# Kernel optimization log

Hardware: AMD Instinct MI355X
Metric: run time of the kernel (lower is better)

The kernel has to match this reference:

```python
import jax, jax.numpy as jnp
import numpy as np

B, C, S = 16, 8, 128
DT, DX, DY = 0.001, 1.0, 1.0
NUM_STEPS = 10
EPS = 1e-6


def _thomas(a, b, c, d):
    """Batched Thomas tridiagonal solve. a,b,c,d: [M,N] rows; solve along N."""
    aT, bT, cT, dT = a.T, b.T, c.T, d.T  # [N, M]
    zero = jnp.zeros_like(dT[0])

    def fwd(carry, inp):
        cs_p, ds_p = carry
        ai, bi, ci, di = inp
        denom = bi - ai * cs_p + EPS  # i=0: cs_p=0 -> denom = b0 + eps (matches torch)
        cs = ci / denom
        ds = (di - ai * ds_p) / denom
        return (cs, ds), (cs, ds)

    _, (c_star, d_star) = jax.lax.scan(fwd, (zero, zero), (aT, bT, cT, dT))

    def bwd(x_next, inp):
        ci, di = inp
        x = di - ci * x_next
        return x, x

    _, xs = jax.lax.scan(bwd, d_star[-1], (c_star[:-1], d_star[:-1]), reverse=True)
    x = jnp.concatenate([xs, d_star[-1:]], axis=0)  # [N, M]
    return x.T


def _diffuse_rows(u2d, coeff):
    """Implicit 1D diffusion along last axis. u2d, coeff: [M,N]."""
    a = -coeff
    c = -coeff
    b = 1.0 + 2.0 * coeff
    b = b.at[:, 0].set(1.0 + coeff[:, 0])
    b = b.at[:, -1].set(1.0 + coeff[:, -1])
    return _thomas(a, b, c, u2d)


def _forward(u, alpha_base, beta_base, alpha_time_coeff, beta_time_coeff, channel_mixing):
    Bb, Cc, H, W = u.shape
    half = DT / 2.0
    t = 0.0
    for _ in range(NUM_STEPS):
        # x half-step (coefficient alpha at time t)
        alpha = jnp.clip(alpha_base + alpha_time_coeff * t, EPS, 10.0)
        u = jnp.einsum('dc,bchw->bdhw', channel_mixing, u)
        uf = u.reshape(Bb * Cc, H, W)
        af = jnp.broadcast_to(alpha[None], (Bb, Cc, H, W)).reshape(Bb * Cc, H, W)
        uf = _diffuse_rows(uf.reshape(-1, W), af.reshape(-1, W) * half / DX**2).reshape(Bb * Cc, H, W)
        t += half
        # y full step (coefficient beta at time t+dt/2)
        beta = jnp.clip(beta_base + beta_time_coeff * t, EPS, 10.0)
        bf = jnp.broadcast_to(beta[None], (Bb, Cc, H, W)).reshape(Bb * Cc, H, W)
        ut = uf.transpose(0, 2, 1).reshape(-1, H)
        bt = bf.transpose(0, 2, 1).reshape(-1, H)
        ut = _diffuse_rows(ut, bt * DT / DY**2)
        uf = ut.reshape(Bb * Cc, W, H).transpose(0, 2, 1)
        t += half
        # x half-step (coefficient alpha at time t+dt)
        alpha = jnp.clip(alpha_base + alpha_time_coeff * t, EPS, 10.0)
        af = jnp.broadcast_to(alpha[None], (Bb, Cc, H, W)).reshape(Bb * Cc, H, W)
        uf = _diffuse_rows(uf.reshape(-1, W), af.reshape(-1, W) * half / DX**2).reshape(Bb * Cc, H, W)
        u = uf.reshape(Bb, Cc, H, W)
    return u


def setup_inputs() -> dict:
    key = jax.random.key(0)
    k_u, k_cm, k_atc, k_btc = jax.random.split(key, 4)
    u = jax.random.normal(k_u, (B, C, S, S), dtype=jnp.float32)
    alpha_base = jnp.ones((C, S, S), dtype=jnp.float32)
    beta_base = jnp.ones((C, S, S), dtype=jnp.float32)
    alpha_time_coeff = jax.random.normal(k_atc, (C, S, S), dtype=jnp.float32) * 0.01
    beta_time_coeff = jax.random.normal(k_btc, (C, S, S), dtype=jnp.float32) * 0.01
    channel_mixing = jnp.eye(C, dtype=jnp.float32) + jax.random.normal(k_cm, (C, C), dtype=jnp.float32) * 0.01
    return {
        'u': u,
        'alpha_base': alpha_base,
        'beta_base': beta_base,
        'alpha_time_coeff': alpha_time_coeff,
        'beta_time_coeff': beta_time_coeff,
        'channel_mixing': channel_mixing,
    }


def reference(u, alpha_base, beta_base, alpha_time_coeff, beta_time_coeff, channel_mixing):
    return _forward(u, alpha_base, beta_base, alpha_time_coeff, beta_time_coeff, channel_mixing)
```

## Files before the change

kernel.cpp:

```cpp
#include <hip/hip_runtime.h>


constexpr int S_ = 128;
constexpr int RS = 129;
constexpr float EPSF = 1e-6f;

constexpr int OFF_A = 0;
constexpr int OFF_B = 12384;
constexpr int OFF_C = 24768;
constexpr int POOL  = 33024;

__device__ __forceinline__ void jrun(const float (&e)[12], const float (&g)[12],
                                     float (&o)[8]) {
    float x1[12];
    #pragma unroll
    for (int i = 1; i <= 10; ++i) x1[i] = fmaf(g[i], e[i - 1] + e[i + 1], e[i]);
    #pragma unroll
    for (int i = 2; i <= 9; ++i) o[i - 2] = fmaf(g[i], x1[i - 1] + x1[i + 1], e[i]);
}

template <bool HEAD, bool TAILMIX>
__global__ __launch_bounds__(512, 2) void step_kernel(
    const float* __restrict__ usrc, float* __restrict__ udst,
    const float* __restrict__ ab, const float* __restrict__ atc,
    const float* __restrict__ bbeta, const float* __restrict__ btc,
    const float* __restrict__ cm, float t_y, float t_x)
{
    __shared__ float sP[POOL];
    const int tid = threadIdx.x;
    const int b   = blockIdx.x >> 4;
    const int h0  = (blockIdx.x & 15) << 3;

    if (HEAD) {
        #pragma unroll
        for (int m = 0; m < 2; ++m) {
            const int col = tid + 512 * m;
            const int c = col >> 7, w = col & 127;
            #pragma unroll
            for (int hh = 0; hh < 12; ++hh) {
                const int gh = h0 - 2 + hh;
                float v = 0.f;
                if (gh >= 0 && gh < S_) v = usrc[((b * 8 + c) * S_ + gh) * S_ + w];
                sP[OFF_A + (c * 12 + hh) * RS + w] = v;
            }
        }
        __syncthreads();
        {
            float M[64];
            #pragma unroll
            for (int i = 0; i < 64; ++i) M[i] = cm[i];
            #pragma unroll
            for (int m = 0; m < 3; ++m) {
                const int p = tid + 512 * m;
                const int hh = p >> 7, w = p & 127;
                float v[8], o[8];
                #pragma unroll
                for (int c = 0; c < 8; ++c) v[c] = sP[OFF_A + (c * 12 + hh) * RS + w];
                #pragma unroll
                for (int dd = 0; dd < 8; ++dd) {
                    float a = 0.f;
                    #pragma unroll
                    for (int c = 0; c < 8; ++c) a = fmaf(M[dd * 8 + c], v[c], a);
                    o[dd] = a;
                }
                #pragma unroll
                for (int c = 0; c < 8; ++c) sP[OFF_A + (c * 12 + hh) * RS + w] = o[c];
            }
        }
        __syncthreads();
        #pragma unroll
        for (int m = 0; m < 3; ++m) {
            const int run = tid + 512 * m;
            const int r96 = run % 96;
            const int wr  = run / 96;
            const int c = r96 / 12, hh = r96 % 12;
            const int gh = h0 - 2 + hh;
            const int w0 = wr * 8;
            const bool rowin = (gh >= 0 && gh < S_);
            float e[12], g[12];
            #pragma unroll
            for (int j = 0; j < 12; ++j) {
                const int wj = w0 - 2 + j;
                const bool win = (wj >= 0 && wj < S_);
                const float dv = win ? sP[OFF_A + r96 * RS + wj] : 0.f;
                float co = 0.f;
                if (rowin && win) {
                    float al = ab[(c * S_ + gh) * S_ + wj];
                    al = fminf(fmaxf(al, EPSF), 10.f);
                    co = al * 0.0005f;
                }
                const float nb = (wj == 0 || wj == S_ - 1) ? 1.f : 2.f;
                const float rb = __builtin_amdgcn_rcpf(fmaf(nb, co, 1.f) + EPSF);
                e[j] = rb * dv; g[j] = rb * co;
            }
            float o[8]; jrun(e, g, o);
            #pragma unroll
            for (int i = 0; i < 8; ++i) sP[OFF_B + r96 * RS + w0 + i] = o[i];
        }
        __syncthreads();
    }

    #pragma unroll
    for (int m = 0; m < 2; ++m) {
        const int col = tid + 512 * m;
        const int c = col >> 7, w = col & 127;
        float e[12], g[12];
        #pragma unroll
        for (int hh = 0; hh < 12; ++hh) {
            const int gh = h0 - 2 + hh;
            const bool inr = (gh >= 0 && gh < S_);
            const int ghc = inr ? gh : 0;
            float dv;
            if (HEAD) dv = sP[OFF_B + (c * 12 + hh) * RS + w];
            else      dv = inr ? usrc[((b * 8 + c) * S_ + ghc) * S_ + w] : 0.f;
            const int gc = (c * S_ + ghc) * S_ + w;
            float be = fmaf(btc[gc], t_y, bbeta[gc]);
            be = fminf(fmaxf(be, EPSF), 10.f);
            const float co = inr ? be * 0.001f : 0.f;
            const float nb = (gh == 0 || gh == S_ - 1) ? 1.f : 2.f;
            const float rb = __builtin_amdgcn_rcpf(fmaf(nb, co, 1.f) + EPSF);
            e[hh] = rb * dv; g[hh] = rb * co;
        }
        float o[8]; jrun(e, g, o);
        #pragma unroll
        for (int i = 0; i < 8; ++i) sP[OFF_A + (c * 8 + i) * RS + w] = o[i];
    }
    #pragma unroll
    for (int m = 0; m < 16; ++m) {
        const int p = tid + 512 * m;
        const int r = p >> 7, w = p & 127;
        const int c = r >> 3, ho = r & 7;
        const int gc = (c * S_ + h0 + ho) * S_ + w;
        float al = fmaf(atc[gc], t_x, ab[gc]);
        al = fminf(fmaxf(al, EPSF), 10.f);
        sP[OFF_C + r * RS + w] = al * 0.0005f;
    }
    __syncthreads();

    float rbk[2][12], gk[2][12], xo[2][8];
    #pragma unroll
    for (int m = 0; m < 2; ++m) {
        const int run = tid + 512 * m;
        const int r = run & 63, wr = run >> 6;
        const int w0 = wr * 8;
        float e[12];
        #pragma unroll
        for (int j = 0; j < 12; ++j) {
            const int wj = w0 - 2 + j;
            const bool win = (wj >= 0 && wj < S_);
            const float co = win ? sP[OFF_C + r * RS + wj] : 0.f;
            const float dv = win ? sP[OFF_A + r * RS + wj] : 0.f;
            const float nb = (wj == 0 || wj == S_ - 1) ? 1.f : 2.f;
            const float rb = __builtin_amdgcn_rcpf(fmaf(nb, co, 1.f) + EPSF);
            rbk[m][j] = rb; gk[m][j] = rb * co;
            e[j] = rb * dv;
        }
        jrun(e, gk[m], xo[m]);
    }

    if (TAILMIX) {
        #pragma unroll
        for (int m = 0; m < 2; ++m) {
            const int run = tid + 512 * m;
            const int r = run & 63, w0 = (run >> 6) * 8;
            #pragma unroll
            for (int i = 0; i < 8; ++i) sP[OFF_B + r * RS + w0 + i] = xo[m][i];
        }
        __syncthreads();
        float M[64];
        #pragma unroll
        for (int i = 0; i < 64; ++i) M[i] = cm[i];
        #pragma unroll
        for (int m = 0; m < 2; ++m) {
            const int p = tid + 512 * m;
            const int ho = p >> 7, w = p & 127;
            float v[8], o[8];
            #pragma unroll
            for (int c = 0; c < 8; ++c) v[c] = sP[OFF_B + (c * 8 + ho) * RS + w];
            #pragma unroll
            for (int dd = 0; dd < 8; ++dd) {
                float a = 0.f;
                #pragma unroll
                for (int c = 0; c < 8; ++c) a = fmaf(M[dd * 8 + c], v[c], a);
                o[dd] = a;
            }
            #pragma unroll
            for (int c = 0; c < 8; ++c) sP[OFF_A + (c * 8 + ho) * RS + w] = o[c];
        }
        __syncthreads();
        #pragma unroll
        for (int m = 0; m < 2; ++m) {
            const int run = tid + 512 * m;
            const int r = run & 63, wr = run >> 6;
            const int w0 = wr * 8;
            const int c = r >> 3, ho = r & 7;
            float e[12];
            #pragma unroll
            for (int j = 0; j < 12; ++j) {
                const int wj = w0 - 2 + j;
                const bool win = (wj >= 0 && wj < S_);
                const float dv = win ? sP[OFF_A + r * RS + wj] : 0.f;
                e[j] = rbk[m][j] * dv;
            }
            float o[8]; jrun(e, gk[m], o);
            float4* dst4 = (float4*)&udst[((b * 8 + c) * S_ + h0 + ho) * S_ + w0];
            dst4[0] = make_float4(o[0], o[1], o[2], o[3]);
            dst4[1] = make_float4(o[4], o[5], o[6], o[7]);
        }
    } else {
        #pragma unroll
        for (int m = 0; m < 2; ++m) {
            const int run = tid + 512 * m;
            const int r = run & 63, wr = run >> 6;
            const int w0 = wr * 8;
            const int c = r >> 3, ho = r & 7;
            float4* dst4 = (float4*)&udst[((b * 8 + c) * S_ + h0 + ho) * S_ + w0];
            dst4[0] = make_float4(xo[m][0], xo[m][1], xo[m][2], xo[m][3]);
            dst4[1] = make_float4(xo[m][4], xo[m][5], xo[m][6], xo[m][7]);
        }
    }
}

extern "C" void kernel_launch(void* const* d_in, const int* in_sizes, int n_in,
                              void* d_out, int out_size, void* d_ws, size_t ws_size,
                              hipStream_t stream) {
    const float* u_in = (const float*)d_in[0];
    const float* ab   = (const float*)d_in[1];
    const float* bbta = (const float*)d_in[2];
    const float* atc  = (const float*)d_in[3];
    const float* btc  = (const float*)d_in[4];
    const float* cm   = (const float*)d_in[5];
    float* uo = (float*)d_out;
    float* uw = (float*)d_ws;

    const dim3 g(256), blk(512);
    const float dt2 = 0.0005f;

    step_kernel<true, true><<<g, blk, 0, stream>>>(u_in, uw, ab, atc, bbta, btc, cm,
                                                   1 * dt2, 2 * dt2);
    const float* src = uw; float* dst = uo;
    for (int k = 1; k <= 8; ++k) {
        step_kernel<false, true><<<g, blk, 0, stream>>>(src, dst, ab, atc, bbta, btc, cm,
                                                        (2 * k + 1) * dt2, (2 * k + 2) * dt2);
        const float* ns = dst; dst = (dst == uo) ? uw : uo; src = ns;
    }
    step_kernel<false, false><<<g, blk, 0, stream>>>(src, dst, ab, atc, bbta, btc, cm,
                                                     19 * dt2, 20 * dt2);
}
```

Measured before the change: 179.3 us.

## Halve row tile per block to double grid and raise occupancy

```diff
diff --git a/kernel.cpp b/kernel.cpp
--- a/kernel.cpp
+++ b/kernel.cpp
@@ -5,31 +5,33 @@
 constexpr int RS = 129;
 constexpr float EPSF = 1e-6f;
 
-constexpr int OFF_A = 0;
-constexpr int OFF_B = 12384;
-constexpr int OFF_C = 24768;
-constexpr int POOL  = 33024;
-
-__device__ __forceinline__ void jrun(const float (&e)[12], const float (&g)[12],
-                                     float (&o)[8]) {
-    float x1[12];
-    #pragma unroll
-    for (int i = 1; i <= 10; ++i) x1[i] = fmaf(g[i], e[i - 1] + e[i + 1], e[i]);
-    #pragma unroll
-    for (int i = 2; i <= 9; ++i) o[i - 2] = fmaf(g[i], x1[i - 1] + x1[i + 1], e[i]);
+constexpr int OFF_X  = 0;
+constexpr int OFF_C  = 32 * RS;
+constexpr int OFF_B  = 64 * RS;
+constexpr int OFF_HA = 96 * RS;
+
+template <int N>
+__device__ __forceinline__ void jrunN(const float (&e)[N], const float (&g)[N],
+                                      float (&o)[N - 4]) {
+    float x1[N];
+    #pragma unroll
+    for (int i = 1; i <= N - 2; ++i) x1[i] = fmaf(g[i], e[i - 1] + e[i + 1], e[i]);
+    #pragma unroll
+    for (int i = 2; i <= N - 3; ++i) o[i - 2] = fmaf(g[i], x1[i - 1] + x1[i + 1], e[i]);
 }
 
 template <bool HEAD, bool TAILMIX>
-__global__ __launch_bounds__(512, 2) void step_kernel(
+__global__ __launch_bounds__(512, 4) void step_kernel(
     const float* __restrict__ usrc, float* __restrict__ udst,
     const float* __restrict__ ab, const float* __restrict__ atc,
     const float* __restrict__ bbeta, const float* __restrict__ btc,
     const float* __restrict__ cm, float t_y, float t_x)
 {
+    constexpr int POOL = HEAD ? 160 * RS : 96 * RS;
     __shared__ float sP[POOL];
     const int tid = threadIdx.x;
-    const int b   = blockIdx.x >> 4;
-    const int h0  = (blockIdx.x & 15) << 3;
+    const int b   = blockIdx.x >> 5;
+    const int h0  = (blockIdx.x & 31) << 2;
 
     if (HEAD) {
         #pragma unroll
@@ -37,11 +39,11 @@
             const int col = tid + 512 * m;
             const int c = col >> 7, w = col & 127;
             #pragma unroll
-            for (int hh = 0; hh < 12; ++hh) {
+            for (int hh = 0; hh < 8; ++hh) {
                 const int gh = h0 - 2 + hh;
                 float v = 0.f;
                 if (gh >= 0 && gh < S_) v = usrc[((b * 8 + c) * S_ + gh) * S_ + w];
-                sP[OFF_A + (c * 12 + hh) * RS + w] = v;
+                sP[(c * 8 + hh) * RS + w] = v;
             }
         }
         __syncthreads();
@@ -50,12 +52,12 @@
             #pragma unroll
             for (int i = 0; i < 64; ++i) M[i] = cm[i];
             #pragma unroll
-            for (int m = 0; m < 3; ++m) {
+            for (int m = 0; m < 2; ++m) {
                 const int p = tid + 512 * m;
                 const int hh = p >> 7, w = p & 127;
                 float v[8], o[8];
                 #pragma unroll
-                for (int c = 0; c < 8; ++c) v[c] = sP[OFF_A + (c * 12 + hh) * RS + w];
+                for (int c = 0; c < 8; ++c) v[c] = sP[(c * 8 + hh) * RS + w];
                 #pragma unroll
                 for (int dd = 0; dd < 8; ++dd) {
                     float a = 0.f;
@@ -64,16 +66,16 @@
                     o[dd] = a;
                 }
                 #pragma unroll
-                for (int c = 0; c < 8; ++c) sP[OFF_A + (c * 12 + hh) * RS + w] = o[c];
-            }
-        }
-        __syncthreads();
-        #pragma unroll
-        for (int m = 0; m < 3; ++m) {
+                for (int c = 0; c < 8; ++c) sP[(c * 8 + hh) * RS + w] = o[c];
+            }
+        }
+        __syncthreads();
+        #pragma unroll
+        for (int m = 0; m < 2; ++m) {
             const int run = tid + 512 * m;
-            const int r96 = run % 96;
-            const int wr  = run / 96;
-            const int c = r96 / 12, hh = r96 % 12;
+            const int r64 = run & 63;
+            const int wr  = run >> 6;
+            const int c = r64 >> 3, hh = r64 & 7;
             const int gh = h0 - 2 + hh;
             const int w0 = wr * 8;
             const bool rowin = (gh >= 0 && gh < S_);
@@ -82,7 +84,7 @@
             for (int j = 0; j < 12; ++j) {
                 const int wj = w0 - 2 + j;
                 const bool win = (wj >= 0 && wj < S_);
-                const float dv = win ? sP[OFF_A + r96 * RS + wj] : 0.f;
+                const float dv = win ? sP[r64 * RS + wj] : 0.f;
                 float co = 0.f;
                 if (rowin && win) {
                     float al = ab[(c * S_ + gh) * S_ + wj];
@@ -93,9 +95,9 @@
                 const float rb = __builtin_amdgcn_rcpf(fmaf(nb, co, 1.f) + EPSF);
                 e[j] = rb * dv; g[j] = rb * co;
             }
-            float o[8]; jrun(e, g, o);
-            #pragma unroll
-            for (int i = 0; i < 8; ++i) sP[OFF_B + r96 * RS + w0 + i] = o[i];
+            float o[8]; jrunN<12>(e, g, o);
+            #pragma unroll
+            for (int i = 0; i < 8; ++i) sP[OFF_HA + r64 * RS + w0 + i] = o[i];
         }
         __syncthreads();
     }
@@ -104,14 +106,14 @@
     for (int m = 0; m < 2; ++m) {
         const int col = tid + 512 * m;
         const int c = col >> 7, w = col & 127;
-        float e[12], g[12];
-        #pragma unroll
-        for (int hh = 0; hh < 12; ++hh) {
+        float e[8], g[8];
+        #pragma unroll
+        for (int hh = 0; hh < 8; ++hh) {
             const int gh = h0 - 2 + hh;
             const bool inr = (gh >= 0 && gh < S_);
             const int ghc = inr ? gh : 0;
             float dv;
-            if (HEAD) dv = sP[OFF_B + (c * 12 + hh) * RS + w];
+            if (HEAD) dv = sP[OFF_HA + (c * 8 + hh) * RS + w];
             else      dv = inr ? usrc[((b * 8 + c) * S_ + ghc) * S_ + w] : 0.f;
             const int gc = (c * S_ + ghc) * S_ + w;
             float be = fmaf(btc[gc], t_y, bbeta[gc]);
@@ -121,15 +123,15 @@
             const float rb = __builtin_amdgcn_rcpf(fmaf(nb, co, 1.f) + EPSF);
             e[hh] = rb * dv; g[hh] = rb * co;
         }
-        float o[8]; jrun(e, g, o);
-        #pragma unroll
-        for (int i = 0; i < 8; ++i) sP[OFF_A + (c * 8 + i) * RS + w] = o[i];
-    }
-    #pragma unroll
-    for (int m = 0; m < 16; ++m) {
+        float o[4]; jrunN<8>(e, g, o);
+        #pragma unroll
+        for (int i = 0; i < 4; ++i) sP[OFF_X + (c * 4 + i) * RS + w] = o[i];
+    }
+    #pragma unroll
+    for (int m = 0; m < 8; ++m) {
         const int p = tid + 512 * m;
         const int r = p >> 7, w = p & 127;
-        const int c = r >> 3, ho = r & 7;
+        const int c = r >> 2, ho = r & 3;
         const int gc = (c * S_ + h0 + ho) * S_ + w;
         float al = fmaf(atc[gc], t_x, ab[gc]);
         al = fminf(fmaxf(al, EPSF), 10.f);
@@ -137,46 +139,37 @@
     }
     __syncthreads();
 
-    float rbk[2][12], gk[2][12], xo[2][8];
-    #pragma unroll
-    for (int m = 0; m < 2; ++m) {
-        const int run = tid + 512 * m;
-        const int r = run & 63, wr = run >> 6;
-        const int w0 = wr * 8;
+    const int r32 = tid & 31, wr = tid >> 5;
+    const int w0 = wr * 8;
+    float rbk[12], gk[12], xo[8];
+    {
         float e[12];
         #pragma unroll
         for (int j = 0; j < 12; ++j) {
             const int wj = w0 - 2 + j;
             const bool win = (wj >= 0 && wj < S_);
-            const float co = win ? sP[OFF_C + r * RS + wj] : 0.f;
-            const float dv = win ? sP[OFF_A + r * RS + wj] : 0.f;
+            const float co = win ? sP[OFF_C + r32 * RS + wj] : 0.f;
+            const float dv = win ? sP[OFF_X + r32 * RS + wj] : 0.f;
             const float nb = (wj == 0 || wj == S_ - 1) ? 1.f : 2.f;
             const float rb = __builtin_amdgcn_rcpf(fmaf(nb, co, 1.f) + EPSF);
-            rbk[m][j] = rb; gk[m][j] = rb * co;
+            rbk[j] = rb; gk[j] = rb * co;
             e[j] = rb * dv;
         }
-        jrun(e, gk[m], xo[m]);
+        jrunN<12>(e, gk, xo);
     }
 
     if (TAILMIX) {
         #pragma unroll
-        for (int m = 0; m < 2; ++m) {
-            const int run = tid + 512 * m;
-            const int r = run & 63, w0 = (run >> 6) * 8;
-            #pragma unroll
-            for (int i = 0; i < 8; ++i) sP[OFF_B + r * RS + w0 + i] = xo[m][i];
-        }
-        __syncthreads();
-        float M[64];
-        #pragma unroll
-        for (int i = 0; i < 64; ++i) M[i] = cm[i];
-        #pragma unroll
-        for (int m = 0; m < 2; ++m) {
-            const int p = tid + 512 * m;
-            const int ho = p >> 7, w = p & 127;
+        for (int i = 0; i < 8; ++i) sP[OFF_B + r32 * RS + w0 + i] = xo[i];
+        __syncthreads();
+        {
+            float M[64];
+            #pragma unroll
+            for (int i = 0; i < 64; ++i) M[i] = cm[i];
+            const int ho = tid >> 7, w = tid & 127;
             float v[8], o[8];
             #pragma unroll
-            for (int c = 0; c < 8; ++c) v[c] = sP[OFF_B + (c * 8 + ho) * RS + w];
+            for (int c = 0; c < 8; ++c) v[c] = sP[OFF_B + (c * 4 + ho) * RS + w];
             #pragma unroll
             for (int dd = 0; dd < 8; ++dd) {
                 float a = 0.f;
@@ -185,39 +178,29 @@
                 o[dd] = a;
             }
             #pragma unroll
-            for (int c = 0; c < 8; ++c) sP[OFF_A + (c * 8 + ho) * RS + w] = o[c];
-        }
-        __syncthreads();
-        #pragma unroll
-        for (int m = 0; m < 2; ++m) {
-            const int run = tid + 512 * m;
-            const int r = run & 63, wr = run >> 6;
-            const int w0 = wr * 8;
-            const int c = r >> 3, ho = r & 7;
+            for (int c = 0; c < 8; ++c) sP[OFF_X + (c * 4 + ho) * RS + w] = o[c];
+        }
+        __syncthreads();
+        {
+            const int c = r32 >> 2, ho = r32 & 3;
             float e[12];
             #pragma unroll
             for (int j = 0; j < 12; ++j) {
                 const int wj = w0 - 2 + j;
                 const bool win = (wj >= 0 && wj < S_);
-                const float dv = win ? sP[OFF_A + r * RS + wj] : 0.f;
-                e[j] = rbk[m][j] * dv;
-            }
-            float o[8]; jrun(e, gk[m], o);
+                const float dv = win ? sP[OFF_X + r32 * RS + wj] : 0.f;
+                e[j] = rbk[j] * dv;
+            }
+            float o[8]; jrunN<12>(e, gk, o);
             float4* dst4 = (float4*)&udst[((b * 8 + c) * S_ + h0 + ho) * S_ + w0];
             dst4[0] = make_float4(o[0], o[1], o[2], o[3]);
             dst4[1] = make_float4(o[4], o[5], o[6], o[7]);
         }
     } else {
-        #pragma unroll
-        for (int m = 0; m < 2; ++m) {
-            const int run = tid + 512 * m;
-            const int r = run & 63, wr = run >> 6;
-            const int w0 = wr * 8;
-            const int c = r >> 3, ho = r & 7;
-            float4* dst4 = (float4*)&udst[((b * 8 + c) * S_ + h0 + ho) * S_ + w0];
-            dst4[0] = make_float4(xo[m][0], xo[m][1], xo[m][2], xo[m][3]);
-            dst4[1] = make_float4(xo[m][4], xo[m][5], xo[m][6], xo[m][7]);
-        }
+        const int c = r32 >> 2, ho = r32 & 3;
+        float4* dst4 = (float4*)&udst[((b * 8 + c) * S_ + h0 + ho) * S_ + w0];
+        dst4[0] = make_float4(xo[0], xo[1], xo[2], xo[3]);
+        dst4[1] = make_float4(xo[4], xo[5], xo[6], xo[7]);
     }
 }
 
@@ -233,7 +216,7 @@
     float* uo = (float*)d_out;
     float* uw = (float*)d_ws;
 
-    const dim3 g(256), blk(512);
+    const dim3 g(512), blk(512);
     const float dt2 = 0.0005f;
 
     step_kernel<true, true><<<g, blk, 0, stream>>>(u_in, uw, ab, atc, bbta, btc, cm,
```

After: 188.0 us. 4.8% more time.

## Fuse ten step launches into one persistent kernel with a grid barrier

Applied to the files above, without the earlier changes.

```diff
diff --git a/kernel.cpp b/kernel.cpp
--- a/kernel.cpp
+++ b/kernel.cpp
@@ -4,11 +4,38 @@
 constexpr int S_ = 128;
 constexpr int RS = 129;
 constexpr float EPSF = 1e-6f;
+constexpr int NBLK = 256;
 
 constexpr int OFF_A = 0;
 constexpr int OFF_B = 12384;
 constexpr int OFF_C = 24768;
 constexpr int POOL  = 33024;
+
+__device__ unsigned g_cnt = 0;
+__device__ unsigned g_gen = 0;
+
+__device__ __forceinline__ void gridbar() {
+    __syncthreads();
+    if (threadIdx.x == 0) {
+        __threadfence();
+        unsigned gen = __hip_atomic_load(&g_gen, __ATOMIC_RELAXED,
+                                         __HIP_MEMORY_SCOPE_AGENT);
+        unsigned old = __hip_atomic_fetch_add(&g_cnt, 1u, __ATOMIC_ACQ_REL,
+                                              __HIP_MEMORY_SCOPE_AGENT);
+        if (old == NBLK - 1) {
+            __hip_atomic_store(&g_cnt, 0u, __ATOMIC_RELAXED,
+                               __HIP_MEMORY_SCOPE_AGENT);
+            __hip_atomic_fetch_add(&g_gen, 1u, __ATOMIC_RELEASE,
+                                   __HIP_MEMORY_SCOPE_AGENT);
+        } else {
+            while (__hip_atomic_load(&g_gen, __ATOMIC_RELAXED,
+                                     __HIP_MEMORY_SCOPE_AGENT) == gen)
+                __builtin_amdgcn_s_sleep(8);
+        }
+        __threadfence();
+    }
+    __syncthreads();
+}
 
 __device__ __forceinline__ void jrun(const float (&e)[12], const float (&g)[12],
                                      float (&o)[8]) {
@@ -19,205 +46,216 @@
     for (int i = 2; i <= 9; ++i) o[i - 2] = fmaf(g[i], x1[i - 1] + x1[i + 1], e[i]);
 }
 
-template <bool HEAD, bool TAILMIX>
-__global__ __launch_bounds__(512, 2) void step_kernel(
-    const float* __restrict__ usrc, float* __restrict__ udst,
+__global__ __launch_bounds__(512, 2) void adi10_kernel(
+    const float* __restrict__ u0, float* __restrict__ bws, float* __restrict__ bout,
     const float* __restrict__ ab, const float* __restrict__ atc,
     const float* __restrict__ bbeta, const float* __restrict__ btc,
-    const float* __restrict__ cm, float t_y, float t_x)
+    const float* __restrict__ cm)
 {
     __shared__ float sP[POOL];
     const int tid = threadIdx.x;
     const int b   = blockIdx.x >> 4;
     const int h0  = (blockIdx.x & 15) << 3;
-
-    if (HEAD) {
+    const float dt2 = 0.0005f;
+
+    for (int k = 0; k < 10; ++k) {
+        const bool head = (k == 0);
+        const bool tailmix = (k < 9);
+        const float t_y = (2 * k + 1) * dt2;
+        const float t_x = (2 * k + 2) * dt2;
+        const float* src = head ? u0 : ((k & 1) ? bws : bout);
+        float* dst = (k & 1) ? bout : bws;
+
+        if (head) {
+            #pragma unroll
+            for (int m = 0; m < 2; ++m) {
+                const int col = tid + 512 * m;
+                const int c = col >> 7, w = col & 127;
+                #pragma unroll
+                for (int hh = 0; hh < 12; ++hh) {
+                    const int gh = h0 - 2 + hh;
+                    float v = 0.f;
+                    if (gh >= 0 && gh < S_) v = u0[((b * 8 + c) * S_ + gh) * S_ + w];
+                    sP[OFF_A + (c * 12 + hh) * RS + w] = v;
+                }
+            }
+            __syncthreads();
+            {
+                float M[64];
+                #pragma unroll
+                for (int i = 0; i < 64; ++i) M[i] = cm[i];
+                #pragma unroll
+                for (int m = 0; m < 3; ++m) {
+                    const int p = tid + 512 * m;
+                    const int hh = p >> 7, w = p & 127;
+                    float v[8], o[8];
+                    #pragma unroll
+                    for (int c = 0; c < 8; ++c) v[c] = sP[OFF_A + (c * 12 + hh) * RS + w];
+                    #pragma unroll
+                    for (int dd = 0; dd < 8; ++dd) {
+                        float a = 0.f;
+                        #pragma unroll
+                        for (int c = 0; c < 8; ++c) a = fmaf(M[dd * 8 + c], v[c], a);
+                        o[dd] = a;
+                    }
+                    #pragma unroll
+                    for (int c = 0; c < 8; ++c) sP[OFF_A + (c * 12 + hh) * RS + w] = o[c];
+                }
+            }
+            __syncthreads();
+            #pragma unroll
+            for (int m = 0; m < 3; ++m) {
+                const int run = tid + 512 * m;
+                const int r96 = run % 96;
+                const int wr  = run / 96;
+                const int c = r96 / 12, hh = r96 % 12;
+                const int gh = h0 - 2 + hh;
+                const int w0 = wr * 8;
+                const bool rowin = (gh >= 0 && gh < S_);
+                float e[12], g[12];
+                #pragma unroll
+                for (int j = 0; j < 12; ++j) {
+                    const int wj = w0 - 2 + j;
+                    const bool win = (wj >= 0 && wj < S_);
+                    const float dv = win ? sP[OFF_A + r96 * RS + wj] : 0.f;
+                    float co = 0.f;
+                    if (rowin && win) {
+                        float al = ab[(c * S_ + gh) * S_ + wj];
+                        al = fminf(fmaxf(al, EPSF), 10.f);
+                        co = al * 0.0005f;
+                    }
+                    const float nb = (wj == 0 || wj == S_ - 1) ? 1.f : 2.f;
+                    const float rb = __builtin_amdgcn_rcpf(fmaf(nb, co, 1.f) + EPSF);
+                    e[j] = rb * dv; g[j] = rb * co;
+                }
+                float o[8]; jrun(e, g, o);
+                #pragma unroll
+                for (int i = 0; i < 8; ++i) sP[OFF_B + r96 * RS + w0 + i] = o[i];
+            }
+            __syncthreads();
+        }
+
         #pragma unroll
         for (int m = 0; m < 2; ++m) {
             const int col = tid + 512 * m;
             const int c = col >> 7, w = col & 127;
+            float e[12], g[12];
             #pragma unroll
             for (int hh = 0; hh < 12; ++hh) {
                 const int gh = h0 - 2 + hh;
-                float v = 0.f;
-                if (gh >= 0 && gh < S_) v = usrc[((b * 8 + c) * S_ + gh) * S_ + w];
-                sP[OFF_A + (c * 12 + hh) * RS + w] = v;
-            }
+                const bool inr = (gh >= 0 && gh < S_);
+                const int ghc = inr ? gh : 0;
+                float dv;
+                if (head) dv = sP[OFF_B + (c * 12 + hh) * RS + w];
+                else      dv = inr ? src[((b * 8 + c) * S_ + ghc) * S_ + w] : 0.f;
+                const int gc = (c * S_ + ghc) * S_ + w;
+                float be = fmaf(btc[gc], t_y, bbeta[gc]);
+                be = fminf(fmaxf(be, EPSF), 10.f);
+                const float co = inr ? be * 0.001f : 0.f;
+                const float nb = (gh == 0 || gh == S_ - 1) ? 1.f : 2.f;
+                const float rb = __builtin_amdgcn_rcpf(fmaf(nb, co, 1.f) + EPSF);
+                e[hh] = rb * dv; g[hh] = rb * co;
+            }
+            float o[8]; jrun(e, g, o);
+            #pragma unroll
+            for (int i = 0; i < 8; ++i) sP[OFF_A + (c * 8 + i) * RS + w] = o[i];
+        }
+        #pragma unroll
+        for (int m = 0; m < 16; ++m) {
+            const int p = tid + 512 * m;
+            const int r = p >> 7, w = p & 127;
+            const int c = r >> 3, ho = r & 7;
+            const int gc = (c * S_ + h0 + ho) * S_ + w;
+            float al = fmaf(atc[gc], t_x, ab[gc]);
+            al = fminf(fmaxf(al, EPSF), 10.f);
+            sP[OFF_C + r * RS + w] = al * 0.0005f;
         }
         __syncthreads();
-        {
-            float M[64];
-            #pragma unroll
-            for (int i = 0; i < 64; ++i) M[i] = cm[i];
-            #pragma unroll
-            for (int m = 0; m < 3; ++m) {
-                const int p = tid + 512 * m;
-                const int hh = p >> 7, w = p & 127;
-                float v[8], o[8];
-                #pragma unroll
-                for (int c = 0; c < 8; ++c) v[c] = sP[OFF_A + (c * 12 + hh) * RS + w];
-                #pragma unroll
-                for (int dd = 0; dd < 8; ++dd) {
-                    float a = 0.f;
-                    #pragma unroll
-                    for (int c = 0; c < 8; ++c) a = fmaf(M[dd * 8 + c], v[c], a);
-                    o[dd] = a;
-                }
-                #pragma unroll
-                for (int c = 0; c < 8; ++c) sP[OFF_A + (c * 12 + hh) * RS + w] = o[c];
-            }
-        }
-        __syncthreads();
-        #pragma unroll
-        for (int m = 0; m < 3; ++m) {
-            const int run = tid + 512 * m;
-            const int r96 = run % 96;
-            const int wr  = run / 96;
-            const int c = r96 / 12, hh = r96 % 12;
-            const int gh = h0 - 2 + hh;
-            const int w0 = wr * 8;
-            const bool rowin = (gh >= 0 && gh < S_);
-            float e[12], g[12];
-            #pragma unroll
-            for (int j = 0; j < 12; ++j) {
-                const int wj = w0 - 2 + j;
-                const bool win = (wj >= 0 && wj < S_);
-                const float dv = win ? sP[OFF_A + r96 * RS + wj] : 0.f;
-                float co = 0.f;
-                if (rowin && win) {
-                    float al = ab[(c * S_ + gh) * S_ + wj];
-                    al = fminf(fmaxf(al, EPSF), 10.f);
-                    co = al * 0.0005f;
-                }
-                const float nb = (wj == 0 || wj == S_ - 1) ? 1.f : 2.f;
-                const float rb = __builtin_amdgcn_rcpf(fmaf(nb, co, 1.f) + EPSF);
-                e[j] = rb * dv; g[j] = rb * co;
-            }
-            float o[8]; jrun(e, g, o);
-            #pragma unroll
-            for (int i = 0; i < 8; ++i) sP[OFF_B + r96 * RS + w0 + i] = o[i];
-        }
-        __syncthreads();
-    }
-
-    #pragma unroll
-    for (int m = 0; m < 2; ++m) {
-        const int col = tid + 512 * m;
-        const int c = col >> 7, w = col & 127;
-        float e[12], g[12];
-        #pragma unroll
-        for (int hh = 0; hh < 12; ++hh) {
-            const int gh = h0 - 2 + hh;
-            const bool inr = (gh >= 0 && gh < S_);
-            const int ghc = inr ? gh : 0;
-            float dv;
-            if (HEAD) dv = sP[OFF_B + (c * 12 + hh) * RS + w];
-            else      dv = inr ? usrc[((b * 8 + c) * S_ + ghc) * S_ + w] : 0.f;
-            const int gc = (c * S_ + ghc) * S_ + w;
-            float be = fmaf(btc[gc], t_y, bbeta[gc]);
-            be = fminf(fmaxf(be, EPSF), 10.f);
-            const float co = inr ? be * 0.001f : 0.f;
-            const float nb = (gh == 0 || gh == S_ - 1) ? 1.f : 2.f;
-            const float rb = __builtin_amdgcn_rcpf(fmaf(nb, co, 1.f) + EPSF);
-            e[hh] = rb * dv; g[hh] = rb * co;
-        }
-        float o[8]; jrun(e, g, o);
-        #pragma unroll
-        for (int i = 0; i < 8; ++i) sP[OFF_A + (c * 8 + i) * RS + w] = o[i];
-    }
-    #pragma unroll
-    for (int m = 0; m < 16; ++m) {
-        const int p = tid + 512 * m;
-        const int r = p >> 7, w = p & 127;
-        const int c = r >> 3, ho = r & 7;
-        const int gc = (c * S_ + h0 + ho) * S_ + w;
-        float al = fmaf(atc[gc], t_x, ab[gc]);
-        al = fminf(fmaxf(al, EPSF), 10.f);
-        sP[OFF_C + r * RS + w] = al * 0.0005f;
-    }
-    __syncthreads();
-
-    float rbk[2][12], gk[2][12], xo[2][8];
-    #pragma unroll
-    for (int m = 0; m < 2; ++m) {
-        const int run = tid + 512 * m;
-        const int r = run & 63, wr = run >> 6;
-        const int w0 = wr * 8;
-        float e[12];
-        #pragma unroll
-        for (int j = 0; j < 12; ++j) {
-            const int wj = w0 - 2 + j;
-            const bool win = (wj >= 0 && wj < S_);
-            const float co = win ? sP[OFF_C + r * RS + wj] : 0.f;
-            const float dv = win ? sP[OFF_A + r * RS + wj] : 0.f;
-            const float nb = (wj == 0 || wj == S_ - 1) ? 1.f : 2.f;
-            const float rb = __builtin_amdgcn_rcpf(fmaf(nb, co, 1.f) + EPSF);
-            rbk[m][j] = rb; gk[m][j] = rb * co;
-            e[j] = rb * dv;
-        }
-        jrun(e, gk[m], xo[m]);
-    }
-
-    if (TAILMIX) {
-        #pragma unroll
-        for (int m = 0; m < 2; ++m) {
-            const int run = tid + 512 * m;
-            const int r = run & 63, w0 = (run >> 6) * 8;
-            #pragma unroll
-            for (int i = 0; i < 8; ++i) sP[OFF_B + r * RS + w0 + i] = xo[m][i];
-        }
-        __syncthreads();
-        float M[64];
-        #pragma unroll
-        for (int i = 0; i < 64; ++i) M[i] = cm[i];
-        #pragma unroll
-        for (int m = 0; m < 2; ++m) {
-            const int p = tid + 512 * m;
-            const int ho = p >> 7, w = p & 127;
-            float v[8], o[8];
-            #pragma unroll
-            for (int c = 0; c < 8; ++c) v[c] = sP[OFF_B + (c * 8 + ho) * RS + w];
-            #pragma unroll
-            for (int dd = 0; dd < 8; ++dd) {
-                float a = 0.f;
-                #pragma unroll
-                for (int c = 0; c < 8; ++c) a = fmaf(M[dd * 8 + c], v[c], a);
-                o[dd] = a;
-            }
-            #pragma unroll
-            for (int c = 0; c < 8; ++c) sP[OFF_A + (c * 8 + ho) * RS + w] = o[c];
-        }
-        __syncthreads();
+
+        float rbk[2][12], gk[2][12], xo[2][8];
         #pragma unroll
         for (int m = 0; m < 2; ++m) {
             const int run = tid + 512 * m;
             const int r = run & 63, wr = run >> 6;
             const int w0 = wr * 8;
-            const int c = r >> 3, ho = r & 7;
             float e[12];
             #pragma unroll
             for (int j = 0; j < 12; ++j) {
                 const int wj = w0 - 2 + j;
                 const bool win = (wj >= 0 && wj < S_);
+                const float co = win ? sP[OFF_C + r * RS + wj] : 0.f;
                 const float dv = win ? sP[OFF_A + r * RS + wj] : 0.f;
-                e[j] = rbk[m][j] * dv;
-            }
-            float o[8]; jrun(e, gk[m], o);
-            float4* dst4 = (float4*)&udst[((b * 8 + c) * S_ + h0 + ho) * S_ + w0];
-            dst4[0] = make_float4(o[0], o[1], o[2], o[3]);
-            dst4[1] = make_float4(o[4], o[5], o[6], o[7]);
-        }
-    } else {
-        #pragma unroll
-        for (int m = 0; m < 2; ++m) {
-            const int run = tid + 512 * m;
-            const int r = run & 63, wr = run >> 6;
-            const int w0 = wr * 8;
-            const int c = r >> 3, ho = r & 7;
-            float4* dst4 = (float4*)&udst[((b * 8 + c) * S_ + h0 + ho) * S_ + w0];
-            dst4[0] = make_float4(xo[m][0], xo[m][1], xo[m][2], xo[m][3]);
-            dst4[1] = make_float4(xo[m][4], xo[m][5], xo[m][6], xo[m][7]);
-        }
+                const float nb = (wj == 0 || wj == S_ - 1) ? 1.f : 2.f;
+                const float rb = __builtin_amdgcn_rcpf(fmaf(nb, co, 1.f) + EPSF);
+                rbk[m][j] = rb; gk[m][j] = rb * co;
+                e[j] = rb * dv;
+            }
+            jrun(e, gk[m], xo[m]);
+        }
+
+        if (tailmix) {
+            #pragma unroll
+            for (int m = 0; m < 2; ++m) {
+                const int run = tid + 512 * m;
+                const int r = run & 63, w0 = (run >> 6) * 8;
+                #pragma unroll
+                for (int i = 0; i < 8; ++i) sP[OFF_B + r * RS + w0 + i] = xo[m][i];
+            }
+            __syncthreads();
+            float M[64];
+            #pragma unroll
+            for (int i = 0; i < 64; ++i) M[i] = cm[i];
+            #pragma unroll
+            for (int m = 0; m < 2; ++m) {
+                const int p = tid + 512 * m;
+                const int ho = p >> 7, w = p & 127;
+                float v[8], o[8];
+                #pragma unroll
+                for (int c = 0; c < 8; ++c) v[c] = sP[OFF_B + (c * 8 + ho) * RS + w];
+                #pragma unroll
+                for (int dd = 0; dd < 8; ++dd) {
+                    float a = 0.f;
+                    #pragma unroll
+                    for (int c = 0; c < 8; ++c) a = fmaf(M[dd * 8 + c], v[c], a);
+                    o[dd] = a;
+                }
+                #pragma unroll
+                for (int c = 0; c < 8; ++c) sP[OFF_A + (c * 8 + ho) * RS + w] = o[c];
+            }
+            __syncthreads();
+            #pragma unroll
+            for (int m = 0; m < 2; ++m) {
+                const int run = tid + 512 * m;
+                const int r = run & 63, wr = run >> 6;
+                const int w0 = wr * 8;
+                const int c = r >> 3, ho = r & 7;
+                float e[12];
+                #pragma unroll
+                for (int j = 0; j < 12; ++j) {
+                    const int wj = w0 - 2 + j;
+                    const bool win = (wj >= 0 && wj < S_);
+                    const float dv = win ? sP[OFF_A + r * RS + wj] : 0.f;
+                    e[j] = rbk[m][j] * dv;
+                }
+                float o[8]; jrun(e, gk[m], o);
+                float4* dst4 = (float4*)&dst[((b * 8 + c) * S_ + h0 + ho) * S_ + w0];
+                dst4[0] = make_float4(o[0], o[1], o[2], o[3]);
+                dst4[1] = make_float4(o[4], o[5], o[6], o[7]);
+            }
+        } else {
+            #pragma unroll
+            for (int m = 0; m < 2; ++m) {
+                const int run = tid + 512 * m;
+                const int r = run & 63, wr = run >> 6;
+                const int w0 = wr * 8;
+                const int c = r >> 3, ho = r & 7;
+                float4* dst4 = (float4*)&dst[((b * 8 + c) * S_ + h0 + ho) * S_ + w0];
+                dst4[0] = make_float4(xo[m][0], xo[m][1], xo[m][2], xo[m][3]);
+                dst4[1] = make_float4(xo[m][4], xo[m][5], xo[m][6], xo[m][7]);
+            }
+        }
+
+        if (k < 9) gridbar();
     }
 }
 
@@ -233,17 +271,6 @@
     float* uo = (float*)d_out;
     float* uw = (float*)d_ws;
 
-    const dim3 g(256), blk(512);
-    const float dt2 = 0.0005f;
-
-    step_kernel<true, true><<<g, blk, 0, stream>>>(u_in, uw, ab, atc, bbta, btc, cm,
-                                                   1 * dt2, 2 * dt2);
-    const float* src = uw; float* dst = uo;
-    for (int k = 1; k <= 8; ++k) {
-        step_kernel<false, true><<<g, blk, 0, stream>>>(src, dst, ab, atc, bbta, btc, cm,
-                                                        (2 * k + 1) * dt2, (2 * k + 2) * dt2);
-        const float* ns = dst; dst = (dst == uo) ? uw : uo; src = ns;
-    }
-    step_kernel<false, false><<<g, blk, 0, stream>>>(src, dst, ab, atc, bbta, btc, cm,
-                                                     19 * dt2, 20 * dt2);
-}
+    adi10_kernel<<<dim3(NBLK), dim3(512), 0, stream>>>(u_in, uw, uo, ab, atc,
+                                                       bbta, btc, cm);
+}
```

Result: slower. 610.6 us (+240.5%).

## Fuse two time steps per kernel with wider halo to halve launches

Applied to the files above, without the earlier changes.

```diff
diff --git a/kernel.cpp b/kernel.cpp
--- a/kernel.cpp
+++ b/kernel.cpp
@@ -5,27 +5,36 @@
 constexpr int RS = 129;
 constexpr float EPSF = 1e-6f;
 
-constexpr int OFF_A = 0;
-constexpr int OFF_B = 12384;
-constexpr int OFF_C = 24768;
-constexpr int POOL  = 33024;
-
-__device__ __forceinline__ void jrun(const float (&e)[12], const float (&g)[12],
-                                     float (&o)[8]) {
-    float x1[12];
-    #pragma unroll
-    for (int i = 1; i <= 10; ++i) x1[i] = fmaf(g[i], e[i - 1] + e[i + 1], e[i]);
-    #pragma unroll
-    for (int i = 2; i <= 9; ++i) o[i - 2] = fmaf(g[i], x1[i - 1] + x1[i + 1], e[i]);
+constexpr int OFF_P  = 0;
+constexpr int OFF_Q  = 96 * RS;
+constexpr int OFF_ST = 96 * RS;
+
+template <int N>
+__device__ __forceinline__ void jrunN(const float (&e)[N], const float (&g)[N],
+                                      float (&o)[N - 4]) {
+    float x1[N];
+    #pragma unroll
+    for (int i = 1; i <= N - 2; ++i) x1[i] = fmaf(g[i], e[i - 1] + e[i + 1], e[i]);
+    #pragma unroll
+    for (int i = 2; i <= N - 3; ++i) o[i - 2] = fmaf(g[i], x1[i - 1] + x1[i + 1], e[i]);
 }
 
-template <bool HEAD, bool TAILMIX>
-__global__ __launch_bounds__(512, 2) void step_kernel(
+__device__ __forceinline__ float xcoef(const float* __restrict__ ab,
+                                       const float* __restrict__ atc,
+                                       int gc, float t) {
+    float al = fmaf(atc[gc], t, ab[gc]);
+    return fminf(fmaxf(al, EPSF), 10.f) * 0.0005f;
+}
+
+template <bool HEAD, bool LAST>
+__global__ __launch_bounds__(512, 2) void pair_kernel(
     const float* __restrict__ usrc, float* __restrict__ udst,
     const float* __restrict__ ab, const float* __restrict__ atc,
     const float* __restrict__ bbeta, const float* __restrict__ btc,
-    const float* __restrict__ cm, float t_y, float t_x)
+    const float* __restrict__ cm,
+    float t_ya, float t_xa, float t_yb, float t_xb)
 {
+    constexpr int POOL = HEAD ? 224 * RS : 192 * RS;
     __shared__ float sP[POOL];
     const int tid = threadIdx.x;
     const int b   = blockIdx.x >> 4;
@@ -37,11 +46,11 @@
             const int col = tid + 512 * m;
             const int c = col >> 7, w = col & 127;
             #pragma unroll
-            for (int hh = 0; hh < 12; ++hh) {
-                const int gh = h0 - 2 + hh;
+            for (int hh = 0; hh < 16; ++hh) {
+                const int gh = h0 - 4 + hh;
                 float v = 0.f;
                 if (gh >= 0 && gh < S_) v = usrc[((b * 8 + c) * S_ + gh) * S_ + w];
-                sP[OFF_A + (c * 12 + hh) * RS + w] = v;
+                sP[OFF_ST + (c * 16 + hh) * RS + w] = v;
             }
         }
         __syncthreads();
@@ -50,12 +59,12 @@
             #pragma unroll
             for (int i = 0; i < 64; ++i) M[i] = cm[i];
             #pragma unroll
-            for (int m = 0; m < 3; ++m) {
+            for (int m = 0; m < 4; ++m) {
                 const int p = tid + 512 * m;
                 const int hh = p >> 7, w = p & 127;
                 float v[8], o[8];
                 #pragma unroll
-                for (int c = 0; c < 8; ++c) v[c] = sP[OFF_A + (c * 12 + hh) * RS + w];
+                for (int c = 0; c < 8; ++c) v[c] = sP[OFF_ST + (c * 16 + hh) * RS + w];
                 #pragma unroll
                 for (int dd = 0; dd < 8; ++dd) {
                     float a = 0.f;
@@ -64,41 +73,147 @@
                     o[dd] = a;
                 }
                 #pragma unroll
-                for (int c = 0; c < 8; ++c) sP[OFF_A + (c * 12 + hh) * RS + w] = o[c];
-            }
-        }
-        __syncthreads();
-        #pragma unroll
-        for (int m = 0; m < 3; ++m) {
-            const int run = tid + 512 * m;
-            const int r96 = run % 96;
-            const int wr  = run / 96;
-            const int c = r96 / 12, hh = r96 % 12;
-            const int gh = h0 - 2 + hh;
+                for (int c = 0; c < 8; ++c) sP[OFF_ST + (c * 16 + hh) * RS + w] = o[c];
+            }
+        }
+        __syncthreads();
+        float xh[4][8];
+        #pragma unroll
+        for (int m = 0; m < 4; ++m) {
+            const int task = tid + 512 * m;
+            const int rr = task & 127, wr = task >> 7;
+            const int c = rr >> 4, hh = rr & 15;
+            const int gh = h0 - 4 + hh;
+            const int ghc = (gh < 0) ? 0 : ((gh >= S_) ? S_ - 1 : gh);
+            const bool rowin = (gh >= 0 && gh < S_);
             const int w0 = wr * 8;
-            const bool rowin = (gh >= 0 && gh < S_);
             float e[12], g[12];
             #pragma unroll
             for (int j = 0; j < 12; ++j) {
                 const int wj = w0 - 2 + j;
                 const bool win = (wj >= 0 && wj < S_);
-                const float dv = win ? sP[OFF_A + r96 * RS + wj] : 0.f;
+                const float dv = win ? sP[OFF_ST + rr * RS + wj] : 0.f;
                 float co = 0.f;
                 if (rowin && win) {
                     float al = ab[(c * S_ + gh) * S_ + wj];
-                    al = fminf(fmaxf(al, EPSF), 10.f);
-                    co = al * 0.0005f;
+                    co = fminf(fmaxf(al, EPSF), 10.f) * 0.0005f;
                 }
                 const float nb = (wj == 0 || wj == S_ - 1) ? 1.f : 2.f;
                 const float rb = __builtin_amdgcn_rcpf(fmaf(nb, co, 1.f) + EPSF);
                 e[j] = rb * dv; g[j] = rb * co;
             }
-            float o[8]; jrun(e, g, o);
-            #pragma unroll
-            for (int i = 0; i < 8; ++i) sP[OFF_B + r96 * RS + w0 + i] = o[i];
-        }
-        __syncthreads();
-    }
+            jrunN<12>(e, g, xh[m]);
+        }
+        __syncthreads();
+        #pragma unroll
+        for (int m = 0; m < 4; ++m) {
+            const int task = tid + 512 * m;
+            const int rr = task & 127, w0 = (task >> 7) * 8;
+            #pragma unroll
+            for (int i = 0; i < 8; ++i) sP[OFF_ST + rr * RS + w0 + i] = xh[m][i];
+        }
+        __syncthreads();
+    }
+
+    #pragma unroll
+    for (int m = 0; m < 2; ++m) {
+        const int col = tid + 512 * m;
+        const int c = col >> 7, w = col & 127;
+        float e[16], g[16];
+        #pragma unroll
+        for (int hh = 0; hh < 16; ++hh) {
+            const int gh = h0 - 4 + hh;
+            const bool inr = (gh >= 0 && gh < S_);
+            const int ghc = inr ? gh : 0;
+            float dv;
+            if (HEAD) dv = sP[OFF_ST + (c * 16 + hh) * RS + w];
+            else      dv = inr ? usrc[((b * 8 + c) * S_ + ghc) * S_ + w] : 0.f;
+            if (HEAD && !inr) dv = 0.f;
+            const int gc = (c * S_ + ghc) * S_ + w;
+            float be = fmaf(btc[gc], t_ya, bbeta[gc]);
+            be = fminf(fmaxf(be, EPSF), 10.f);
+            const float co = inr ? be * 0.001f : 0.f;
+            const float nb = (gh == 0 || gh == S_ - 1) ? 1.f : 2.f;
+            const float rb = __builtin_amdgcn_rcpf(fmaf(nb, co, 1.f) + EPSF);
+            e[hh] = rb * dv; g[hh] = rb * co;
+        }
+        float o[12]; jrunN<16>(e, g, o);
+        #pragma unroll
+        for (int i = 0; i < 12; ++i) sP[OFF_P + (c * 12 + i) * RS + w] = o[i];
+    }
+    __syncthreads();
+
+    #pragma unroll
+    for (int m = 0; m < 3; ++m) {
+        const int task = tid + 512 * m;
+        const int rr = task % 96, wr = task / 96;
+        const int c = rr / 12, ha = rr % 12;
+        const int gh = h0 - 2 + ha;
+        const int ghc = (gh < 0) ? 0 : ((gh >= S_) ? S_ - 1 : gh);
+        const int w0 = wr * 8;
+        float e[12], g[12];
+        #pragma unroll
+        for (int j = 0; j < 12; ++j) {
+            const int wj = w0 - 2 + j;
+            const bool win = (wj >= 0 && wj < S_);
+            const float dv = win ? sP[OFF_P + rr * RS + wj] : 0.f;
+            const float co = win ? xcoef(ab, atc, (c * S_ + ghc) * S_ + wj, t_xa) : 0.f;
+            const float nb = (wj == 0 || wj == S_ - 1) ? 1.f : 2.f;
+            const float rb = __builtin_amdgcn_rcpf(fmaf(nb, co, 1.f) + EPSF);
+            e[j] = rb * dv; g[j] = rb * co;
+        }
+        float o[8]; jrunN<12>(e, g, o);
+        #pragma unroll
+        for (int i = 0; i < 8; ++i) sP[OFF_Q + rr * RS + w0 + i] = o[i];
+    }
+    __syncthreads();
+    {
+        float M[64];
+        #pragma unroll
+        for (int i = 0; i < 64; ++i) M[i] = cm[i];
+        #pragma unroll
+        for (int m = 0; m < 3; ++m) {
+            const int p = tid + 512 * m;
+            const int ha = p >> 7, w = p & 127;
+            float v[8], o[8];
+            #pragma unroll
+            for (int c = 0; c < 8; ++c) v[c] = sP[OFF_Q + (c * 12 + ha) * RS + w];
+            #pragma unroll
+            for (int dd = 0; dd < 8; ++dd) {
+                float a = 0.f;
+                #pragma unroll
+                for (int c = 0; c < 8; ++c) a = fmaf(M[dd * 8 + c], v[c], a);
+                o[dd] = a;
+            }
+            #pragma unroll
+            for (int c = 0; c < 8; ++c) sP[OFF_Q + (c * 12 + ha) * RS + w] = o[c];
+        }
+    }
+    __syncthreads();
+    #pragma unroll
+    for (int m = 0; m < 3; ++m) {
+        const int task = tid + 512 * m;
+        const int rr = task % 96, wr = task / 96;
+        const int c = rr / 12, ha = rr % 12;
+        const int gh = h0 - 2 + ha;
+        const int ghc = (gh < 0) ? 0 : ((gh >= S_) ? S_ - 1 : gh);
+        const int w0 = wr * 8;
+        float e[12], g[12];
+        #pragma unroll
+        for (int j = 0; j < 12; ++j) {
+            const int wj = w0 - 2 + j;
+            const bool win = (wj >= 0 && wj < S_);
+            const float dv = win ? sP[OFF_Q + rr * RS + wj] : 0.f;
+            const float co = win ? xcoef(ab, atc, (c * S_ + ghc) * S_ + wj, t_xa) : 0.f;
+            const float nb = (wj == 0 || wj == S_ - 1) ? 1.f : 2.f;
+            const float rb = __builtin_amdgcn_rcpf(fmaf(nb, co, 1.f) + EPSF);
+            e[j] = rb * dv; g[j] = rb * co;
+        }
+        float o[8]; jrunN<12>(e, g, o);
+        #pragma unroll
+        for (int i = 0; i < 8; ++i) sP[OFF_P + rr * RS + w0 + i] = o[i];
+    }
+    __syncthreads();
 
     #pragma unroll
     for (int m = 0; m < 2; ++m) {
@@ -110,61 +225,60 @@
             const int gh = h0 - 2 + hh;
             const bool inr = (gh >= 0 && gh < S_);
             const int ghc = inr ? gh : 0;
-            float dv;
-            if (HEAD) dv = sP[OFF_B + (c * 12 + hh) * RS + w];
-            else      dv = inr ? usrc[((b * 8 + c) * S_ + ghc) * S_ + w] : 0.f;
+            const float dv = inr ? sP[OFF_P + (c * 12 + hh) * RS + w] : 0.f;
             const int gc = (c * S_ + ghc) * S_ + w;
-            float be = fmaf(btc[gc], t_y, bbeta[gc]);
+            float be = fmaf(btc[gc], t_yb, bbeta[gc]);
             be = fminf(fmaxf(be, EPSF), 10.f);
             const float co = inr ? be * 0.001f : 0.f;
             const float nb = (gh == 0 || gh == S_ - 1) ? 1.f : 2.f;
             const float rb = __builtin_amdgcn_rcpf(fmaf(nb, co, 1.f) + EPSF);
             e[hh] = rb * dv; g[hh] = rb * co;
         }
-        float o[8]; jrun(e, g, o);
-        #pragma unroll
-        for (int i = 0; i < 8; ++i) sP[OFF_A + (c * 8 + i) * RS + w] = o[i];
-    }
-    #pragma unroll
-    for (int m = 0; m < 16; ++m) {
-        const int p = tid + 512 * m;
-        const int r = p >> 7, w = p & 127;
+        float o[8]; jrunN<12>(e, g, o);
+        #pragma unroll
+        for (int i = 0; i < 8; ++i) sP[OFF_Q + (c * 8 + i) * RS + w] = o[i];
+    }
+    __syncthreads();
+
+    float xo[2][8];
+    #pragma unroll
+    for (int m = 0; m < 2; ++m) {
+        const int task = tid + 512 * m;
+        const int r = task & 63, wr = task >> 6;
         const int c = r >> 3, ho = r & 7;
-        const int gc = (c * S_ + h0 + ho) * S_ + w;
-        float al = fmaf(atc[gc], t_x, ab[gc]);
-        al = fminf(fmaxf(al, EPSF), 10.f);
-        sP[OFF_C + r * RS + w] = al * 0.0005f;
-    }
-    __syncthreads();
-
-    float rbk[2][12], gk[2][12], xo[2][8];
-    #pragma unroll
-    for (int m = 0; m < 2; ++m) {
-        const int run = tid + 512 * m;
-        const int r = run & 63, wr = run >> 6;
+        const int gh = h0 + ho;
         const int w0 = wr * 8;
-        float e[12];
+        float e[12], g[12];
         #pragma unroll
         for (int j = 0; j < 12; ++j) {
             const int wj = w0 - 2 + j;
             const bool win = (wj >= 0 && wj < S_);
-            const float co = win ? sP[OFF_C + r * RS + wj] : 0.f;
-            const float dv = win ? sP[OFF_A + r * RS + wj] : 0.f;
+            const float dv = win ? sP[OFF_Q + r * RS + wj] : 0.f;
+            const float co = win ? xcoef(ab, atc, (c * S_ + gh) * S_ + wj, t_xb) : 0.f;
             const float nb = (wj == 0 || wj == S_ - 1) ? 1.f : 2.f;
             const float rb = __builtin_amdgcn_rcpf(fmaf(nb, co, 1.f) + EPSF);
-            rbk[m][j] = rb; gk[m][j] = rb * co;
-            e[j] = rb * dv;
-        }
-        jrun(e, gk[m], xo[m]);
-    }
-
-    if (TAILMIX) {
-        #pragma unroll
-        for (int m = 0; m < 2; ++m) {
-            const int run = tid + 512 * m;
-            const int r = run & 63, w0 = (run >> 6) * 8;
-            #pragma unroll
-            for (int i = 0; i < 8; ++i) sP[OFF_B + r * RS + w0 + i] = xo[m][i];
+            e[j] = rb * dv; g[j] = rb * co;
+        }
+        jrunN<12>(e, g, xo[m]);
+    }
+
+    if (LAST) {
+        #pragma unroll
+        for (int m = 0; m < 2; ++m) {
+            const int task = tid + 512 * m;
+            const int r = task & 63, wr = task >> 6;
+            const int c = r >> 3, ho = r & 7;
+            float4* dst4 = (float4*)&udst[((b * 8 + c) * S_ + h0 + ho) * S_ + wr * 8];
+            dst4[0] = make_float4(xo[m][0], xo[m][1], xo[m][2], xo[m][3]);
+            dst4[1] = make_float4(xo[m][4], xo[m][5], xo[m][6], xo[m][7]);
+        }
+    } else {
+        #pragma unroll
+        for (int m = 0; m < 2; ++m) {
+            const int task = tid + 512 * m;
+            const int r = task & 63, w0 = (task >> 6) * 8;
+            #pragma unroll
+            for (int i = 0; i < 8; ++i) sP[OFF_P + r * RS + w0 + i] = xo[m][i];
         }
         __syncthreads();
         float M[64];
@@ -176,7 +290,7 @@
             const int ho = p >> 7, w = p & 127;
             float v[8], o[8];
             #pragma unroll
-            for (int c = 0; c < 8; ++c) v[c] = sP[OFF_B + (c * 8 + ho) * RS + w];
+            for (int c = 0; c < 8; ++c) v[c] = sP[OFF_P + (c * 8 + ho) * RS + w];
             #pragma unroll
             for (int dd = 0; dd < 8; ++dd) {
                 float a = 0.f;
@@ -185,38 +299,31 @@
                 o[dd] = a;
             }
             #pragma unroll
-            for (int c = 0; c < 8; ++c) sP[OFF_A + (c * 8 + ho) * RS + w] = o[c];
-        }
-        __syncthreads();
-        #pragma unroll
-        for (int m = 0; m < 2; ++m) {
-            const int run = tid + 512 * m;
-            const int r = run & 63, wr = run >> 6;
+            for (int c = 0; c < 8; ++c) sP[OFF_P + (c * 8 + ho) * RS + w] = o[c];
+        }
+        __syncthreads();
+        #pragma unroll
+        for (int m = 0; m < 2; ++m) {
+            const int task = tid + 512 * m;
+            const int r = task & 63, wr = task >> 6;
+            const int c = r >> 3, ho = r & 7;
+            const int gh = h0 + ho;
             const int w0 = wr * 8;
-            const int c = r >> 3, ho = r & 7;
-            float e[12];
+            float e[12], g[12];
             #pragma unroll
             for (int j = 0; j < 12; ++j) {
                 const int wj = w0 - 2 + j;
                 const bool win = (wj >= 0 && wj < S_);
-                const float dv = win ? sP[OFF_A + r * RS + wj] : 0.f;
-                e[j] = rbk[m][j] * dv;
-            }
-            float o[8]; jrun(e, gk[m], o);
-            float4* dst4 = (float4*)&udst[((b * 8 + c) * S_ + h0 + ho) * S_ + w0];
+                const float dv = win ? sP[OFF_P + r * RS + wj] : 0.f;
+                const float co = win ? xcoef(ab, atc, (c * S_ + gh) * S_ + wj, t_xb) : 0.f;
+                const float nb = (wj == 0 || wj == S_ - 1) ? 1.f : 2.f;
+                const float rb = __builtin_amdgcn_rcpf(fmaf(nb, co, 1.f) + EPSF);
+                e[j] = rb * dv; g[j] = rb * co;
+            }
+            float o[8]; jrunN<12>(e, g, o);
+            float4* dst4 = (float4*)&udst[((b * 8 + c) * S_ + gh) * S_ + w0];
             dst4[0] = make_float4(o[0], o[1], o[2], o[3]);
             dst4[1] = make_float4(o[4], o[5], o[6], o[7]);
-        }
-    } else {
-        #pragma unroll
-        for (int m = 0; m < 2; ++m) {
-            const int run = tid + 512 * m;
-            const int r = run & 63, wr = run >> 6;
-            const int w0 = wr * 8;
-            const int c = r >> 3, ho = r & 7;
-            float4* dst4 = (float4*)&udst[((b * 8 + c) * S_ + h0 + ho) * S_ + w0];
-            dst4[0] = make_float4(xo[m][0], xo[m][1], xo[m][2], xo[m][3]);
-            dst4[1] = make_float4(xo[m][4], xo[m][5], xo[m][6], xo[m][7]);
         }
     }
 }
@@ -230,20 +337,20 @@
     const float* atc  = (const float*)d_in[3];
     const float* btc  = (const float*)d_in[4];
     const float* cm   = (const float*)d_in[5];
-    float* uo = (float*)d_out;
-    float* uw = (float*)d_ws;
+    float* uo  = (float*)d_out;
+    float* uw1 = (float*)d_ws;
+    float* uw2 = (float*)d_ws + (16 * 8 * 128 * 128);
 
     const dim3 g(256), blk(512);
     const float dt2 = 0.0005f;
-
-    step_kernel<true, true><<<g, blk, 0, stream>>>(u_in, uw, ab, atc, bbta, btc, cm,
-                                                   1 * dt2, 2 * dt2);
-    const float* src = uw; float* dst = uo;
-    for (int k = 1; k <= 8; ++k) {
-        step_kernel<false, true><<<g, blk, 0, stream>>>(src, dst, ab, atc, bbta, btc, cm,
-                                                        (2 * k + 1) * dt2, (2 * k + 2) * dt2);
-        const float* ns = dst; dst = (dst == uo) ? uw : uo; src = ns;
-    }
-    step_kernel<false, false><<<g, blk, 0, stream>>>(src, dst, ab, atc, bbta, btc, cm,
-                                                     19 * dt2, 20 * dt2);
+    pair_kernel<true, false><<<g, blk, 0, stream>>>(u_in, uw1, ab, atc, bbta, btc, cm,
+                                                    1 * dt2, 2 * dt2, 3 * dt2, 4 * dt2);
+    pair_kernel<false, false><<<g, blk, 0, stream>>>(uw1, uw2, ab, atc, bbta, btc, cm,
+                                                     5 * dt2, 6 * dt2, 7 * dt2, 8 * dt2);
+    pair_kernel<false, false><<<g, blk, 0, stream>>>(uw2, uw1, ab, atc, bbta, btc, cm,
+                                                     9 * dt2, 10 * dt2, 11 * dt2, 12 * dt2);
+    pair_kernel<false, false><<<g, blk, 0, stream>>>(uw1, uw2, ab, atc, bbta, btc, cm,
+                                                     13 * dt2, 14 * dt2, 15 * dt2, 16 * dt2);
+    pair_kernel<false, true><<<g, blk, 0, stream>>>(uw2, uo, ab, atc, bbta, btc, cm,
+                                                    17 * dt2, 18 * dt2, 19 * dt2, 20 * dt2);
 }
```

Result: slower. 332.8 us (+85.6%).
